# Optimization experiments

Hardware: AMD Instinct MI355X
Metric: run time of the kernel (lower is better)

## Reference

```python
import jax, jax.numpy as jnp
import numpy as np

B, TQ, TV = 16, 2048, 2048
DEC, ENC = 1024, 512

def setup_inputs() -> dict:
    key = jax.random.key(0)
    k1, k2, k3 = jax.random.split(key, 3)
    query = jax.random.normal(k1, (B, TQ, DEC), dtype=jnp.float32)
    value = jax.random.normal(k2, (B, TV, ENC), dtype=jnp.float32)
    # Dense(decoder_dim): kernel [ENC, DEC] + bias [DEC]
    W = jax.random.normal(k3, (ENC, DEC), dtype=jnp.float32) * (1.0 / np.sqrt(ENC))
    b = jnp.zeros((DEC,), dtype=jnp.float32)
    return {"query": query, "value": value, "W": W, "b": b}

def reference(query, value, W, b):
    # w(value): [B, TV, DEC]
    keys = jnp.einsum('bve,ed->bvd', value, W) + b
    # scores: query @ keys^T -> [B, TQ, TV]
    scores = jnp.einsum('bqd,bvd->bqv', query, keys)
    alignment = jax.nn.softmax(scores, axis=-1)
    # context: alignment @ value -> [B, TQ, ENC]
    context = jnp.einsum('bqv,bve->bqe', alignment, value)
    context = jnp.concatenate([context, query], axis=-1)  # [B, TQ, ENC+DEC]
    alignment_t = jnp.transpose(alignment, (0, 2, 1))      # [B, TV, TQ]
    return (context, alignment_t)
```

## Files before the change

kernel.cpp:

```cpp
#include <hip/hip_runtime.h>
#include <cstdint>
#include <cstddef>

typedef unsigned short u16;
typedef __bf16 bf16x8 __attribute__((ext_vector_type(8)));
typedef unsigned short u16x8 __attribute__((ext_vector_type(8)));
typedef unsigned short u16x4 __attribute__((ext_vector_type(4)));
typedef float f32x4 __attribute__((ext_vector_type(4)));

#define NB   16
#define TQ   2048
#define TV   2048
#define DDEC 1024
#define DENC 512
#define CTXW (DENC + DDEC)
#define CTXW2 (2*CTXW)

static __device__ __forceinline__ u16 f2bf(float f) {
    unsigned u = __builtin_bit_cast(unsigned, f);
    return (u16)((u + 0x7fffu + ((u >> 16) & 1u)) >> 16);
}
static __device__ __forceinline__ float bf2f(u16 h) {
    return __builtin_bit_cast(float, ((unsigned)h) << 16);
}

static __device__ __forceinline__ void stage_tile(
    u16* __restrict__ lds_tile, const u16* __restrict__ gsrc,
    int ldb, int w, int lane)
{
    #pragma unroll
    for (int p = 0; p < 2; ++p) {
        const int ci  = p * 4 + w;
        const int row = ci * 16 + (lane >> 2);
        const int col = (lane & 3) * 8;
        const u16* g = gsrc + (size_t)row * ldb + col;
        u16* l = lds_tile + ci * 512;
        __builtin_amdgcn_global_load_lds(
            (const __attribute__((address_space(1))) void*)g,
            (__attribute__((address_space(3))) void*)l, 16, 0, 0);
    }
}

__global__ __launch_bounds__(256)
void lk_prep_split(const float* __restrict__ X, u16* __restrict__ Xh, u16* __restrict__ Xl)
{
    const size_t i = ((size_t)blockIdx.x * 256 + threadIdx.x) * 4;
    const float4 v = *(const float4*)(X + i);
    const u16 h0=f2bf(v.x), h1=f2bf(v.y), h2=f2bf(v.z), h3=f2bf(v.w);
    u16x4 hv = {h0,h1,h2,h3};
    u16x4 lv = {f2bf(v.x-bf2f(h0)), f2bf(v.y-bf2f(h1)),
                f2bf(v.z-bf2f(h2)), f2bf(v.w-bf2f(h3))};
    *(u16x4*)(Xh + i) = hv;
    *(u16x4*)(Xl + i) = lv;
}

__global__ __launch_bounds__(256)
void lk_prep_v(const float* __restrict__ V, u16* __restrict__ Vh,
               u16* __restrict__ Vl, u16* __restrict__ Vt)
{
    __shared__ float ts[32][36];
    const int t = threadIdx.x;
    const int r = t >> 3, c = (t & 7) * 4;
    const int e0 = blockIdx.x * 32, v0 = blockIdx.y * 32;
    const size_t bin  = (size_t)blockIdx.z * TV * DENC;
    const float4 v = *(const float4*)(V + bin + (size_t)(v0 + r) * DENC + e0 + c);
    *(float4*)&ts[r][c] = v;
    const u16 h0=f2bf(v.x), h1=f2bf(v.y), h2=f2bf(v.z), h3=f2bf(v.w);
    u16x4 hv = {h0,h1,h2,h3};
    u16x4 lv = {f2bf(v.x-bf2f(h0)), f2bf(v.y-bf2f(h1)),
                f2bf(v.z-bf2f(h2)), f2bf(v.w-bf2f(h3))};
    *(u16x4*)(Vh + bin + (size_t)(v0 + r) * DENC + e0 + c) = hv;
    *(u16x4*)(Vl + bin + (size_t)(v0 + r) * DENC + e0 + c) = lv;
    __syncthreads();
    u16x4 tv;
    #pragma unroll
    for (int x = 0; x < 4; ++x) tv[x] = f2bf(ts[c + x][r]);
    *(u16x4*)(Vt + (size_t)blockIdx.z * DENC * TV + (size_t)(e0 + r) * TV + v0 + c) = tv;
}

__global__ __launch_bounds__(256)
void lk_gemm_qw(const u16* __restrict__ Ah_g, const u16* __restrict__ Al_g,
                const u16* __restrict__ Bh_g, const u16* __restrict__ Bl_g,
                u16* __restrict__ Chi, u16* __restrict__ Clo)
{
    __shared__ u16 lAh[128*32], lAl[128*32], lBh[128*32], lBl[128*32];
    const int m0 = blockIdx.x * 128, n0 = blockIdx.y * 128;
    const int t = threadIdx.x;
    const int w = t >> 6, lane = t & 63, l15 = lane & 15, quad = lane >> 4;

    const u16* Ab_h = Ah_g + (size_t)m0 * DDEC;
    const u16* Ab_l = Al_g + (size_t)m0 * DDEC;
    const u16* Bb_h = Bh_g + (size_t)n0 * DDEC;
    const u16* Bb_l = Bl_g + (size_t)n0 * DDEC;

    f32x4 acc[2][8];
    #pragma unroll
    for (int i = 0; i < 2; ++i)
        #pragma unroll
        for (int j = 0; j < 8; ++j) acc[i][j] = (f32x4){0.f,0.f,0.f,0.f};

    for (int k0 = 0; k0 < DDEC; k0 += 32) {
        stage_tile(lAh, Ab_h + k0, DDEC, w, lane);
        stage_tile(lAl, Ab_l + k0, DDEC, w, lane);
        stage_tile(lBh, Bb_h + k0, DDEC, w, lane);
        stage_tile(lBl, Bb_l + k0, DDEC, w, lane);
        __syncthreads();
        bf16x8 ah[2], al[2];
        #pragma unroll
        for (int tm = 0; tm < 2; ++tm) {
            const int row = w*32 + tm*16 + l15;
            ah[tm] = __builtin_bit_cast(bf16x8, *(const u16x8*)&lAh[row*32 + quad*8]);
            al[tm] = __builtin_bit_cast(bf16x8, *(const u16x8*)&lAl[row*32 + quad*8]);
        }
        #pragma unroll
        for (int tn = 0; tn < 8; ++tn) {
            const int col = tn*16 + l15;
            const bf16x8 bh = __builtin_bit_cast(bf16x8, *(const u16x8*)&lBh[col*32 + quad*8]);
            const bf16x8 bl = __builtin_bit_cast(bf16x8, *(const u16x8*)&lBl[col*32 + quad*8]);
            #pragma unroll
            for (int tm = 0; tm < 2; ++tm) {
                acc[tm][tn] = __builtin_amdgcn_mfma_f32_16x16x32_bf16(ah[tm], bh, acc[tm][tn], 0,0,0);
                acc[tm][tn] = __builtin_amdgcn_mfma_f32_16x16x32_bf16(ah[tm], bl, acc[tm][tn], 0,0,0);
                acc[tm][tn] = __builtin_amdgcn_mfma_f32_16x16x32_bf16(al[tm], bh, acc[tm][tn], 0,0,0);
            }
        }
        __syncthreads();
    }
    #pragma unroll
    for (int tn = 0; tn < 8; ++tn) {
        const int col = n0 + tn*16 + l15;
        #pragma unroll
        for (int tm = 0; tm < 2; ++tm)
            #pragma unroll
            for (int r = 0; r < 4; ++r) {
                const int row = m0 + w*32 + tm*16 + quad*4 + r;
                const float c = acc[tm][tn][r];
                const u16 h = f2bf(c);
                Chi[(size_t)row*DENC + col] = h;
                Clo[(size_t)row*DENC + col] = f2bf(c - bf2f(h));
            }
    }
}

__global__ __launch_bounds__(256)
void lk_gemm_scores(const u16* __restrict__ Ah_g, const u16* __restrict__ Al_g,
                    const u16* __restrict__ Bh_g, const u16* __restrict__ Bl_g,
                    float* __restrict__ Sc)
{
    __shared__ u16 lAh[128*32], lAl[128*32], lBh[128*32], lBl[128*32];
    const int b = blockIdx.z;
    const int m0 = blockIdx.x * 128, n0 = blockIdx.y * 128;
    const int t = threadIdx.x;
    const int w = t >> 6, lane = t & 63, l15 = lane & 15, quad = lane >> 4;

    const u16* Ab_h = Ah_g + (size_t)b * TQ * DENC + (size_t)m0 * DENC;
    const u16* Ab_l = Al_g + (size_t)b * TQ * DENC + (size_t)m0 * DENC;
    const u16* Bb_h = Bh_g + (size_t)b * TV * DENC + (size_t)n0 * DENC;
    const u16* Bb_l = Bl_g + (size_t)b * TV * DENC + (size_t)n0 * DENC;

    f32x4 acc[2][8];
    #pragma unroll
    for (int i = 0; i < 2; ++i)
        #pragma unroll
        for (int j = 0; j < 8; ++j) acc[i][j] = (f32x4){0.f,0.f,0.f,0.f};

    for (int k0 = 0; k0 < DENC; k0 += 32) {
        stage_tile(lAh, Ab_h + k0, DENC, w, lane);
        stage_tile(lAl, Ab_l + k0, DENC, w, lane);
        stage_tile(lBh, Bb_h + k0, DENC, w, lane);
        stage_tile(lBl, Bb_l + k0, DENC, w, lane);
        __syncthreads();
        bf16x8 ah[2], al[2];
        #pragma unroll
        for (int tm = 0; tm < 2; ++tm) {
            const int row = w*32 + tm*16 + l15;
            ah[tm] = __builtin_bit_cast(bf16x8, *(const u16x8*)&lAh[row*32 + quad*8]);
            al[tm] = __builtin_bit_cast(bf16x8, *(const u16x8*)&lAl[row*32 + quad*8]);
        }
        #pragma unroll
        for (int tn = 0; tn < 8; ++tn) {
            const int col = tn*16 + l15;
            const bf16x8 bh = __builtin_bit_cast(bf16x8, *(const u16x8*)&lBh[col*32 + quad*8]);
            const bf16x8 bl = __builtin_bit_cast(bf16x8, *(const u16x8*)&lBl[col*32 + quad*8]);
            #pragma unroll
            for (int tm = 0; tm < 2; ++tm) {
                acc[tm][tn] = __builtin_amdgcn_mfma_f32_16x16x32_bf16(ah[tm], bh, acc[tm][tn], 0,0,0);
                acc[tm][tn] = __builtin_amdgcn_mfma_f32_16x16x32_bf16(ah[tm], bl, acc[tm][tn], 0,0,0);
                acc[tm][tn] = __builtin_amdgcn_mfma_f32_16x16x32_bf16(al[tm], bh, acc[tm][tn], 0,0,0);
            }
        }
        __syncthreads();
    }
    float* Sb = Sc + (size_t)b * TQ * TV;
    #pragma unroll
    for (int tm = 0; tm < 2; ++tm)
        #pragma unroll
        for (int tn = 0; tn < 8; ++tn) {
            const int col = n0 + tn*16 + l15;
            #pragma unroll
            for (int r = 0; r < 4; ++r) {
                const int row = m0 + w*32 + tm*16 + quad*4 + r;
                Sb[(size_t)row*TV + col] = acc[tm][tn][r];
            }
        }
}

__global__ __launch_bounds__(256)
void lk_softmax(float* __restrict__ S, u16* __restrict__ Pbf)
{
    const size_t row = blockIdx.x;
    float* p = S + row * TV;
    u16* pb = Pbf + row * CTXW2 + 2*DENC;
    const int t = threadIdx.x;
    const float4 v0 = *(const float4*)(p + 4*t);
    const float4 v1 = *(const float4*)(p + 1024 + 4*t);
    float mx = fmaxf(fmaxf(fmaxf(v0.x, v0.y), fmaxf(v0.z, v0.w)),
                     fmaxf(fmaxf(v1.x, v1.y), fmaxf(v1.z, v1.w)));
    #pragma unroll
    for (int off = 32; off > 0; off >>= 1) mx = fmaxf(mx, __shfl_xor(mx, off, 64));
    __shared__ float sred[4];
    const int w = t >> 6;
    if ((t & 63) == 0) sred[w] = mx;
    __syncthreads();
    mx = fmaxf(fmaxf(sred[0], sred[1]), fmaxf(sred[2], sred[3]));
    __syncthreads();
    float e[8];
    e[0]=__expf(v0.x-mx); e[1]=__expf(v0.y-mx); e[2]=__expf(v0.z-mx); e[3]=__expf(v0.w-mx);
    e[4]=__expf(v1.x-mx); e[5]=__expf(v1.y-mx); e[6]=__expf(v1.z-mx); e[7]=__expf(v1.w-mx);
    float s = ((e[0]+e[1])+(e[2]+e[3])) + ((e[4]+e[5])+(e[6]+e[7]));
    #pragma unroll
    for (int off = 32; off > 0; off >>= 1) s += __shfl_xor(s, off, 64);
    if ((t & 63) == 0) sred[w] = s;
    __syncthreads();
    s = (sred[0]+sred[1]) + (sred[2]+sred[3]);
    const float inv = 1.0f / s;
    float4 o0 = {e[0]*inv, e[1]*inv, e[2]*inv, e[3]*inv};
    float4 o1 = {e[4]*inv, e[5]*inv, e[6]*inv, e[7]*inv};
    *(float4*)(p + 4*t) = o0;
    *(float4*)(p + 1024 + 4*t) = o1;
    u16x4 b0 = {f2bf(o0.x), f2bf(o0.y), f2bf(o0.z), f2bf(o0.w)};
    u16x4 b1 = {f2bf(o1.x), f2bf(o1.y), f2bf(o1.z), f2bf(o1.w)};
    *(u16x4*)(pb + 4*t) = b0;
    *(u16x4*)(pb + 1024 + 4*t) = b1;
}

__global__ __launch_bounds__(256)
void lk_gemm_ctx(const u16* __restrict__ Vt, float* C)
{
    __shared__ u16 lA[128*32], lB[128*32];
    const int b = blockIdx.z;
    const int m0 = blockIdx.x * 128, n0 = blockIdx.y * 128;
    const int t = threadIdx.x;
    const int w = t >> 6, lane = t & 63, l15 = lane & 15, quad = lane >> 4;

    const u16* Pb = (const u16*)C + ((size_t)b * TQ + m0) * CTXW2 + 2*DENC;
    const u16* Bb = Vt + (size_t)b * DENC * TV + (size_t)n0 * TV;

    f32x4 acc[2][8];
    #pragma unroll
    for (int i = 0; i < 2; ++i)
        #pragma unroll
        for (int j = 0; j < 8; ++j) acc[i][j] = (f32x4){0.f,0.f,0.f,0.f};

    for (int k0 = 0; k0 < TV; k0 += 32) {
        stage_tile(lA, Pb + k0, CTXW2, w, lane);
        stage_tile(lB, Bb + k0, TV, w, lane);
        __syncthreads();
        bf16x8 af[2];
        #pragma unroll
        for (int tm = 0; tm < 2; ++tm) {
            const int row = w*32 + tm*16 + l15;
            af[tm] = __builtin_bit_cast(bf16x8, *(const u16x8*)&lA[row*32 + quad*8]);
        }
        #pragma unroll
        for (int tn = 0; tn < 8; ++tn) {
            const int col = tn*16 + l15;
            const bf16x8 bf = __builtin_bit_cast(bf16x8, *(const u16x8*)&lB[col*32 + quad*8]);
            #pragma unroll
            for (int tm = 0; tm < 2; ++tm)
                acc[tm][tn] = __builtin_amdgcn_mfma_f32_16x16x32_bf16(af[tm], bf, acc[tm][tn], 0,0,0);
        }
        __syncthreads();
    }
    float* Cb = C + (size_t)b * TQ * CTXW;
    #pragma unroll
    for (int tm = 0; tm < 2; ++tm)
        #pragma unroll
        for (int tn = 0; tn < 8; ++tn) {
            const int col = n0 + tn*16 + l15;
            #pragma unroll
            for (int r = 0; r < 4; ++r) {
                const int row = m0 + w*32 + tm*16 + quad*4 + r;
                Cb[(size_t)row*CTXW + col] = acc[tm][tn][r];
            }
        }
}

__global__ __launch_bounds__(256)
void lk_copy_q(const float* __restrict__ Q, float* __restrict__ C)
{
    const size_t idx = (size_t)blockIdx.x * 256 + threadIdx.x;
    const int d4 = (int)(idx & 255);
    const size_t row = idx >> 8;
    const float4 v = *(const float4*)(Q + (row << 10) + 4*d4);
    *(float4*)(C + row * CTXW + DENC + 4*d4) = v;
}

__global__ __launch_bounds__(256)
void lk_transpose(float* __restrict__ A)
{
    const int i = blockIdx.x, j = blockIdx.y;
    if (j < i) return;
    float* Ab = A + (size_t)blockIdx.z * TQ * TV;
    __shared__ float ta[32][36], tb[32][36];
    const int t = threadIdx.x;
    const int r = t >> 3, c = (t & 7) * 4;
    float* pij = Ab + (size_t)(i*32) * TV + j*32;
    float* pji = Ab + (size_t)(j*32) * TV + i*32;
    const float4 va = *(const float4*)(pij + (size_t)r * TV + c);
    *(float4*)&ta[r][c] = va;
    if (i != j) {
        const float4 vb = *(const float4*)(pji + (size_t)r * TV + c);
        *(float4*)&tb[r][c] = vb;
    }
    __syncthreads();
    float4 oa = { ta[c+0][r], ta[c+1][r], ta[c+2][r], ta[c+3][r] };
    *(float4*)(pji + (size_t)r * TV + c) = oa;
    if (i != j) {
        float4 ob = { tb[c+0][r], tb[c+1][r], tb[c+2][r], tb[c+3][r] };
        *(float4*)(pij + (size_t)r * TV + c) = ob;
    }
}

extern "C" void kernel_launch(void* const* d_in, const int* in_sizes, int n_in,
                              void* d_out, int out_size, void* d_ws, size_t ws_size,
                              hipStream_t stream)
{
    (void)in_sizes; (void)n_in; (void)out_size; (void)ws_size;
    const float* Q = (const float*)d_in[0];
    const float* V = (const float*)d_in[1];
    const float* W = (const float*)d_in[2];
    float* out = (float*)d_out;

    float* ctx   = out;
    float* align = out + (size_t)NB * TQ * CTXW;

    u16* q2h = (u16*)ctx;
    u16* q2l = q2h + (size_t)NB * TQ * DENC;
    u16* vsh = q2l + (size_t)NB * TQ * DENC;
    u16* vsl = vsh + (size_t)NB * TV * DENC;

    u16* qh = (u16*)align;
    u16* ql = qh + (size_t)NB * TQ * DDEC;

    u16* wh = (u16*)d_ws;
    u16* wl = wh + (size_t)DENC * DDEC;
    u16* vt = wl + (size_t)DENC * DDEC;

    lk_prep_split<<<DENC*DDEC/1024, 256, 0, stream>>>(W, wh, wl);
    lk_prep_split<<<(size_t)NB*TQ*DDEC/1024, 256, 0, stream>>>(Q, qh, ql);
    lk_prep_v<<<dim3(DENC/32, TV/32, NB), 256, 0, stream>>>(V, vsh, vsl, vt);
    lk_gemm_qw<<<dim3(NB*TQ/128, DENC/128), 256, 0, stream>>>(qh, ql, wh, wl, q2h, q2l);
    lk_gemm_scores<<<dim3(TQ/128, TV/128, NB), 256, 0, stream>>>(q2h, q2l, vsh, vsl, align);
    lk_softmax<<<NB*TQ, 256, 0, stream>>>(align, (u16*)ctx);
    lk_gemm_ctx<<<dim3(TQ/128, DENC/128, NB), 256, 0, stream>>>(vt, ctx);
    lk_copy_q<<<NB*TQ*DDEC/1024, 256, 0, stream>>>(Q, ctx);
    lk_transpose<<<dim3(TV/32, TV/32, NB), 256, 0, stream>>>(align);
}
```

Measured before the change: 1.334 ms.

## Fuse softmax statistics into scores GEMM and normalization into transpose pass

The scores GEMM epilogue now computes per-tile row max and sum-of-exp partials, a small combine kernel merges the 16 column-tile partials per row, and the transpose kernel applies exp/normalize while transposing and also writes the bf16 probabilities. This removes the separate softmax pass, one full read and write of the 16×2048×2048 fp32 score matrix. V prep is split so the stats buffer can alias the Vt workspace before Vt is built. The cost is extra exp work in the GEMM epilogue and a more complex launch order that depends on the workspace aliasing.

```diff
diff --git a/kernel.cpp b/kernel.cpp
--- a/kernel.cpp
+++ b/kernel.cpp
@@ -55,26 +55,18 @@
 }
 
 __global__ __launch_bounds__(256)
-void lk_prep_v(const float* __restrict__ V, u16* __restrict__ Vh,
-               u16* __restrict__ Vl, u16* __restrict__ Vt)
+void lk_prep_vt(const float* __restrict__ V, u16* __restrict__ Vt)
 {
     __shared__ float ts[32][36];
     const int t = threadIdx.x;
     const int r = t >> 3, c = (t & 7) * 4;
     const int e0 = blockIdx.x * 32, v0 = blockIdx.y * 32;
-    const size_t bin  = (size_t)blockIdx.z * TV * DENC;
-    const float4 v = *(const float4*)(V + bin + (size_t)(v0 + r) * DENC + e0 + c);
+    const float* Vb = V + (size_t)blockIdx.z * TV * DENC;
+    const float4 v = *(const float4*)(Vb + (size_t)(v0 + r) * DENC + e0 + c);
     *(float4*)&ts[r][c] = v;
-    const u16 h0=f2bf(v.x), h1=f2bf(v.y), h2=f2bf(v.z), h3=f2bf(v.w);
-    u16x4 hv = {h0,h1,h2,h3};
-    u16x4 lv = {f2bf(v.x-bf2f(h0)), f2bf(v.y-bf2f(h1)),
-                f2bf(v.z-bf2f(h2)), f2bf(v.w-bf2f(h3))};
-    *(u16x4*)(Vh + bin + (size_t)(v0 + r) * DENC + e0 + c) = hv;
-    *(u16x4*)(Vl + bin + (size_t)(v0 + r) * DENC + e0 + c) = lv;
     __syncthreads();
-    u16x4 tv;
-    #pragma unroll
-    for (int x = 0; x < 4; ++x) tv[x] = f2bf(ts[c + x][r]);
+    u16x4 tv = { f2bf(ts[c+0][r]), f2bf(ts[c+1][r]),
+                 f2bf(ts[c+2][r]), f2bf(ts[c+3][r]) };
     *(u16x4*)(Vt + (size_t)blockIdx.z * DENC * TV + (size_t)(e0 + r) * TV + v0 + c) = tv;
 }
 
@@ -145,7 +137,7 @@
 __global__ __launch_bounds__(256)
 void lk_gemm_scores(const u16* __restrict__ Ah_g, const u16* __restrict__ Al_g,
                     const u16* __restrict__ Bh_g, const u16* __restrict__ Bl_g,
-                    float* __restrict__ Sc)
+                    float* __restrict__ Sc, float2* __restrict__ sst)
 {
     __shared__ u16 lAh[128*32], lAl[128*32], lBh[128*32], lBl[128*32];
     const int b = blockIdx.z;
@@ -203,125 +195,79 @@
                 Sb[(size_t)row*TV + col] = acc[tm][tn][r];
             }
         }
-}
-
-__global__ __launch_bounds__(256)
-void lk_softmax(float* __restrict__ S, u16* __restrict__ Pbf)
-{
-    const size_t row = blockIdx.x;
-    float* p = S + row * TV;
-    u16* pb = Pbf + row * CTXW2 + 2*DENC;
-    const int t = threadIdx.x;
-    const float4 v0 = *(const float4*)(p + 4*t);
-    const float4 v1 = *(const float4*)(p + 1024 + 4*t);
-    float mx = fmaxf(fmaxf(fmaxf(v0.x, v0.y), fmaxf(v0.z, v0.w)),
-                     fmaxf(fmaxf(v1.x, v1.y), fmaxf(v1.z, v1.w)));
-    #pragma unroll
-    for (int off = 32; off > 0; off >>= 1) mx = fmaxf(mx, __shfl_xor(mx, off, 64));
-    __shared__ float sred[4];
-    const int w = t >> 6;
-    if ((t & 63) == 0) sred[w] = mx;
-    __syncthreads();
-    mx = fmaxf(fmaxf(sred[0], sred[1]), fmaxf(sred[2], sred[3]));
-    __syncthreads();
-    float e[8];
-    e[0]=__expf(v0.x-mx); e[1]=__expf(v0.y-mx); e[2]=__expf(v0.z-mx); e[3]=__expf(v0.w-mx);
-    e[4]=__expf(v1.x-mx); e[5]=__expf(v1.y-mx); e[6]=__expf(v1.z-mx); e[7]=__expf(v1.w-mx);
-    float s = ((e[0]+e[1])+(e[2]+e[3])) + ((e[4]+e[5])+(e[6]+e[7]));
-    #pragma unroll
-    for (int off = 32; off > 0; off >>= 1) s += __shfl_xor(s, off, 64);
-    if ((t & 63) == 0) sred[w] = s;
-    __syncthreads();
-    s = (sred[0]+sred[1]) + (sred[2]+sred[3]);
-    const float inv = 1.0f / s;
-    float4 o0 = {e[0]*inv, e[1]*inv, e[2]*inv, e[3]*inv};
-    float4 o1 = {e[4]*inv, e[5]*inv, e[6]*inv, e[7]*inv};
-    *(float4*)(p + 4*t) = o0;
-    *(float4*)(p + 1024 + 4*t) = o1;
-    u16x4 b0 = {f2bf(o0.x), f2bf(o0.y), f2bf(o0.z), f2bf(o0.w)};
-    u16x4 b1 = {f2bf(o1.x), f2bf(o1.y), f2bf(o1.z), f2bf(o1.w)};
-    *(u16x4*)(pb + 4*t) = b0;
-    *(u16x4*)(pb + 1024 + 4*t) = b1;
-}
-
-__global__ __launch_bounds__(256)
-void lk_gemm_ctx(const u16* __restrict__ Vt, float* C)
-{
-    __shared__ u16 lA[128*32], lB[128*32];
-    const int b = blockIdx.z;
-    const int m0 = blockIdx.x * 128, n0 = blockIdx.y * 128;
-    const int t = threadIdx.x;
-    const int w = t >> 6, lane = t & 63, l15 = lane & 15, quad = lane >> 4;
-
-    const u16* Pb = (const u16*)C + ((size_t)b * TQ + m0) * CTXW2 + 2*DENC;
-    const u16* Bb = Vt + (size_t)b * DENC * TV + (size_t)n0 * TV;
-
-    f32x4 acc[2][8];
-    #pragma unroll
-    for (int i = 0; i < 2; ++i)
-        #pragma unroll
-        for (int j = 0; j < 8; ++j) acc[i][j] = (f32x4){0.f,0.f,0.f,0.f};
-
-    for (int k0 = 0; k0 < TV; k0 += 32) {
-        stage_tile(lA, Pb + k0, CTXW2, w, lane);
-        stage_tile(lB, Bb + k0, TV, w, lane);
-        __syncthreads();
-        bf16x8 af[2];
-        #pragma unroll
-        for (int tm = 0; tm < 2; ++tm) {
-            const int row = w*32 + tm*16 + l15;
-            af[tm] = __builtin_bit_cast(bf16x8, *(const u16x8*)&lA[row*32 + quad*8]);
-        }
-        #pragma unroll
-        for (int tn = 0; tn < 8; ++tn) {
-            const int col = tn*16 + l15;
-            const bf16x8 bf = __builtin_bit_cast(bf16x8, *(const u16x8*)&lB[col*32 + quad*8]);
-            #pragma unroll
-            for (int tm = 0; tm < 2; ++tm)
-                acc[tm][tn] = __builtin_amdgcn_mfma_f32_16x16x32_bf16(af[tm], bf, acc[tm][tn], 0,0,0);
-        }
-        __syncthreads();
-    }
-    float* Cb = C + (size_t)b * TQ * CTXW;
+    const int by = blockIdx.y;
     #pragma unroll
     for (int tm = 0; tm < 2; ++tm)
         #pragma unroll
-        for (int tn = 0; tn < 8; ++tn) {
-            const int col = n0 + tn*16 + l15;
-            #pragma unroll
-            for (int r = 0; r < 4; ++r) {
+        for (int r = 0; r < 4; ++r) {
+            float m = acc[tm][0][r];
+            #pragma unroll
+            for (int tn = 1; tn < 8; ++tn) m = fmaxf(m, acc[tm][tn][r]);
+            #pragma unroll
+            for (int off = 1; off < 16; off <<= 1) m = fmaxf(m, __shfl_xor(m, off, 64));
+            float s = 0.f;
+            #pragma unroll
+            for (int tn = 0; tn < 8; ++tn) s += __expf(acc[tm][tn][r] - m);
+            #pragma unroll
+            for (int off = 1; off < 16; off <<= 1) s += __shfl_xor(s, off, 64);
+            if (l15 == 0) {
                 const int row = m0 + w*32 + tm*16 + quad*4 + r;
-                Cb[(size_t)row*CTXW + col] = acc[tm][tn][r];
-            }
-        }
-}
-
-__global__ __launch_bounds__(256)
-void lk_copy_q(const float* __restrict__ Q, float* __restrict__ C)
-{
-    const size_t idx = (size_t)blockIdx.x * 256 + threadIdx.x;
-    const int d4 = (int)(idx & 255);
-    const size_t row = idx >> 8;
-    const float4 v = *(const float4*)(Q + (row << 10) + 4*d4);
-    *(float4*)(C + row * CTXW + DENC + 4*d4) = v;
-}
-
-__global__ __launch_bounds__(256)
-void lk_transpose(float* __restrict__ A)
+                sst[((size_t)(b*16 + by))*TQ + row] = (float2){m, s};
+            }
+        }
+}
+
+__global__ __launch_bounds__(256)
+void lk_combine(float2* __restrict__ sst)
+{
+    const int rg = blockIdx.x * 256 + threadIdx.x;
+    const int b = rg >> 11, q = rg & (TQ - 1);
+    float2* base = sst + (size_t)b * 16 * TQ;
+    float2 v[16];
+    float mx = -3.0e38f;
+    #pragma unroll
+    for (int y = 0; y < 16; ++y) {
+        v[y] = base[(size_t)y * TQ + q];
+        mx = fmaxf(mx, v[y].x);
+    }
+    float s = 0.f;
+    #pragma unroll
+    for (int y = 0; y < 16; ++y) s += v[y].y * __expf(v[y].x - mx);
+    base[q] = (float2){mx, 1.0f / s};
+}
+
+__global__ __launch_bounds__(256)
+void lk_norm_t(float* __restrict__ A, float* __restrict__ C,
+               const float2* __restrict__ sstF)
 {
     const int i = blockIdx.x, j = blockIdx.y;
     if (j < i) return;
-    float* Ab = A + (size_t)blockIdx.z * TQ * TV;
+    const int b = blockIdx.z;
+    float* Ab = A + (size_t)b * TQ * TV;
+    u16* Pb = (u16*)C + (size_t)b * TQ * CTXW2 + 2*DENC;
+    const float2* st = sstF + (size_t)b * 16 * TQ;
     __shared__ float ta[32][36], tb[32][36];
     const int t = threadIdx.x;
     const int r = t >> 3, c = (t & 7) * 4;
     float* pij = Ab + (size_t)(i*32) * TV + j*32;
     float* pji = Ab + (size_t)(j*32) * TV + i*32;
-    const float4 va = *(const float4*)(pij + (size_t)r * TV + c);
-    *(float4*)&ta[r][c] = va;
+    {
+        const float2 s2 = st[i*32 + r];
+        const float4 va = *(const float4*)(pij + (size_t)r * TV + c);
+        float4 e = { __expf(va.x - s2.x) * s2.y, __expf(va.y - s2.x) * s2.y,
+                     __expf(va.z - s2.x) * s2.y, __expf(va.w - s2.x) * s2.y };
+        *(float4*)&ta[r][c] = e;
+        u16x4 pv = {f2bf(e.x), f2bf(e.y), f2bf(e.z), f2bf(e.w)};
+        *(u16x4*)(Pb + (size_t)(i*32 + r) * CTXW2 + j*32 + c) = pv;
+    }
     if (i != j) {
+        const float2 s2 = st[j*32 + r];
         const float4 vb = *(const float4*)(pji + (size_t)r * TV + c);
-        *(float4*)&tb[r][c] = vb;
+        float4 e = { __expf(vb.x - s2.x) * s2.y, __expf(vb.y - s2.x) * s2.y,
+                     __expf(vb.z - s2.x) * s2.y, __expf(vb.w - s2.x) * s2.y };
+        *(float4*)&tb[r][c] = e;
+        u16x4 pv = {f2bf(e.x), f2bf(e.y), f2bf(e.z), f2bf(e.w)};
+        *(u16x4*)(Pb + (size_t)(j*32 + r) * CTXW2 + i*32 + c) = pv;
     }
     __syncthreads();
     float4 oa = { ta[c+0][r], ta[c+1][r], ta[c+2][r], ta[c+3][r] };
@@ -332,6 +278,68 @@
     }
 }
 
+__global__ __launch_bounds__(256)
+void lk_gemm_ctx(const u16* __restrict__ Vt, float* C)
+{
+    __shared__ u16 lA[128*32], lB[128*32];
+    const int b = blockIdx.z;
+    const int m0 = blockIdx.x * 128, n0 = blockIdx.y * 128;
+    const int t = threadIdx.x;
+    const int w = t >> 6, lane = t & 63, l15 = lane & 15, quad = lane >> 4;
+
+    const u16* Pb = (const u16*)C + ((size_t)b * TQ + m0) * CTXW2 + 2*DENC;
+    const u16* Bb = Vt + (size_t)b * DENC * TV + (size_t)n0 * TV;
+
+    f32x4 acc[2][8];
+    #pragma unroll
+    for (int i = 0; i < 2; ++i)
+        #pragma unroll
+        for (int j = 0; j < 8; ++j) acc[i][j] = (f32x4){0.f,0.f,0.f,0.f};
+
+    for (int k0 = 0; k0 < TV; k0 += 32) {
+        stage_tile(lA, Pb + k0, CTXW2, w, lane);
+        stage_tile(lB, Bb + k0, TV, w, lane);
+        __syncthreads();
+        bf16x8 af[2];
+        #pragma unroll
+        for (int tm = 0; tm < 2; ++tm) {
+            const int row = w*32 + tm*16 + l15;
+            af[tm] = __builtin_bit_cast(bf16x8, *(const u16x8*)&lA[row*32 + quad*8]);
+        }
+        #pragma unroll
+        for (int tn = 0; tn < 8; ++tn) {
+            const int col = tn*16 + l15;
+            const bf16x8 bf = __builtin_bit_cast(bf16x8, *(const u16x8*)&lB[col*32 + quad*8]);
+            #pragma unroll
+            for (int tm = 0; tm < 2; ++tm)
+                acc[tm][tn] = __builtin_amdgcn_mfma_f32_16x16x32_bf16(af[tm], bf, acc[tm][tn], 0,0,0);
+        }
+        __syncthreads();
+    }
+    float* Cb = C + (size_t)b * TQ * CTXW;
+    #pragma unroll
+    for (int tm = 0; tm < 2; ++tm)
+        #pragma unroll
+        for (int tn = 0; tn < 8; ++tn) {
+            const int col = n0 + tn*16 + l15;
+            #pragma unroll
+            for (int r = 0; r < 4; ++r) {
+                const int row = m0 + w*32 + tm*16 + quad*4 + r;
+                Cb[(size_t)row*CTXW + col] = acc[tm][tn][r];
+            }
+        }
+}
+
+__global__ __launch_bounds__(256)
+void lk_copy_q(const float* __restrict__ Q, float* __restrict__ C)
+{
+    const size_t idx = (size_t)blockIdx.x * 256 + threadIdx.x;
+    const int d4 = (int)(idx & 255);
+    const size_t row = idx >> 8;
+    const float4 v = *(const float4*)(Q + (row << 10) + 4*d4);
+    *(float4*)(C + row * CTXW + DENC + 4*d4) = v;
+}
+
 extern "C" void kernel_launch(void* const* d_in, const int* in_sizes, int n_in,
                               void* d_out, int out_size, void* d_ws, size_t ws_size,
                               hipStream_t stream)
@@ -356,14 +364,16 @@
     u16* wh = (u16*)d_ws;
     u16* wl = wh + (size_t)DENC * DDEC;
     u16* vt = wl + (size_t)DENC * DDEC;
+    float2* sst = (float2*)vt;
 
     lk_prep_split<<<DENC*DDEC/1024, 256, 0, stream>>>(W, wh, wl);
-    lk_prep_split<<<(size_t)NB*TQ*DDEC/1024, 256, 0, stream>>>(Q, qh, ql);
-    lk_prep_v<<<dim3(DENC/32, TV/32, NB), 256, 0, stream>>>(V, vsh, vsl, vt);
+    lk_prep_split<<<NB*TQ*DDEC/1024, 256, 0, stream>>>(Q, qh, ql);
+    lk_prep_split<<<NB*TV*DENC/1024, 256, 0, stream>>>(V, vsh, vsl);
     lk_gemm_qw<<<dim3(NB*TQ/128, DENC/128), 256, 0, stream>>>(qh, ql, wh, wl, q2h, q2l);
-    lk_gemm_scores<<<dim3(TQ/128, TV/128, NB), 256, 0, stream>>>(q2h, q2l, vsh, vsl, align);
-    lk_softmax<<<NB*TQ, 256, 0, stream>>>(align, (u16*)ctx);
+    lk_gemm_scores<<<dim3(TQ/128, TV/128, NB), 256, 0, stream>>>(q2h, q2l, vsh, vsl, align, sst);
+    lk_combine<<<NB*TQ/256, 256, 0, stream>>>(sst);
+    lk_norm_t<<<dim3(TV/32, TV/32, NB), 256, 0, stream>>>(align, ctx, sst);
+    lk_prep_vt<<<dim3(DENC/32, TV/32, NB), 256, 0, stream>>>(V, vt);
     lk_gemm_ctx<<<dim3(TQ/128, DENC/128, NB), 256, 0, stream>>>(vt, ctx);
     lk_copy_q<<<NB*TQ*DDEC/1024, 256, 0, stream>>>(Q, ctx);
-    lk_transpose<<<dim3(TV/32, TV/32, NB), 256, 0, stream>>>(align);
-}
+}
```

Measured after the change: 1.294 ms. 1.03x faster.
